# Kernel tuning notes

Hardware: AMD Instinct MI355X
Metric: run time of the kernel (lower is better)

## Reference

```python
import jax, jax.numpy as jnp
import numpy as np

B, S, D_MODEL, H = 2, 2048, 1024, 16
HD = D_MODEL // H  # 64
THETA = 10000.0


def setup_inputs() -> dict:
    key = jax.random.key(0)
    ks = jax.random.split(key, 5)
    std = (2.0 / (D_MODEL + D_MODEL)) ** 0.5
    x = jax.random.normal(ks[0], (B, S, D_MODEL), dtype=jnp.float32)
    Wq = jax.random.normal(ks[1], (D_MODEL, D_MODEL), dtype=jnp.float32) * std
    Wk = jax.random.normal(ks[2], (D_MODEL, D_MODEL), dtype=jnp.float32) * std
    Wv = jax.random.normal(ks[3], (D_MODEL, D_MODEL), dtype=jnp.float32) * std
    Wo = jax.random.normal(ks[4], (D_MODEL, D_MODEL), dtype=jnp.float32) * std
    # RoPE tables (buffers)
    pos = jnp.arange(S, dtype=jnp.float32)
    freq = THETA ** (-jnp.arange(0, HD, 2, dtype=jnp.float32) / HD)  # [HD/2]
    ang = jnp.outer(pos, freq)  # [S, HD/2]
    token_positions = jnp.arange(S, dtype=jnp.int32)
    return {
        "x": x,
        "token_positions": token_positions,
        "use_rope": 1,
        "Wq": Wq, "Wk": Wk, "Wv": Wv, "Wo": Wo,
        "cos": jnp.cos(ang), "sin": jnp.sin(ang),
    }


def _apply_rope(t, c, sn):
    # t: [b,h,s,d]; c,sn: [s,d/2] (broadcast over b,h)
    e = t[..., 0::2]
    o = t[..., 1::2]
    return jnp.stack([e * c - o * sn, o * c + e * sn], axis=-1).reshape(t.shape)


def reference(x, token_positions, use_rope, Wq, Wk, Wv, Wo, cos, sin):
    b, s, _ = x.shape

    def split_heads(t):  # [b,s,D] -> [b,h,s,hd]
        return t.reshape(b, s, H, HD).transpose(0, 2, 1, 3)

    q = split_heads(x @ Wq.T)
    k = split_heads(x @ Wk.T)
    v = split_heads(x @ Wv.T)

    if use_rope:
        c = cos[token_positions]   # [s, hd/2]
        sn = sin[token_positions]  # [s, hd/2]
        q = _apply_rope(q, c, sn)
        k = _apply_rope(k, c, sn)

    scale = 1.0 / jnp.sqrt(jnp.float32(HD))
    scores = jnp.einsum('bhqd,bhkd->bhqk', q, k) * scale  # [b,h,s,s]
    causal = jnp.tril(jnp.ones((s, s), dtype=bool))
    scores = jnp.where(causal, scores, -jnp.inf)
    attn = jax.nn.softmax(scores, axis=-1)
    y = jnp.einsum('bhqk,bhkd->bhqd', attn, v)
    y = y.transpose(0, 2, 1, 3).reshape(b, s, D_MODEL)
    return y @ Wo.T
```

## Files before the change

### kernel.cpp

```cpp
#include <hip/hip_runtime.h>
#include <math.h>

#define BB 2
#define SS 2048
#define DM 1024
#define NH 16
#define HD 64

typedef __attribute__((ext_vector_type(8))) __bf16 bf16x8;
typedef __attribute__((ext_vector_type(4))) __bf16 bf16x4;
typedef __attribute__((ext_vector_type(8))) unsigned short u16x8;
typedef __attribute__((ext_vector_type(4))) float f32x4;
typedef unsigned short u16;
typedef unsigned int u32;
typedef __attribute__((address_space(1))) unsigned int u32g;
typedef __attribute__((address_space(3))) unsigned int u32l;

#define CEXP 0.18033688011112042f

static __device__ __forceinline__ u16 f2bf(float f) {
    __bf16 h = (__bf16)f;
    return __builtin_bit_cast(unsigned short, h);
}

static __device__ __forceinline__ void gld16(const u16* g, u16* l) {
    __builtin_amdgcn_global_load_lds((const u32g*)g, (u32l*)l, 16, 0, 0);
}

__global__ __launch_bounds__(256)
void cast_all(const float* __restrict__ x,
              const float* __restrict__ wq, const float* __restrict__ wk,
              const float* __restrict__ wv, const float* __restrict__ wo,
              u16* __restrict__ xb, u16* __restrict__ wqb, u16* __restrict__ wkb,
              u16* __restrict__ wvb, u16* __restrict__ wob)
{
    const int N4X = (BB * SS * DM) / 4;
    const int N4W = (DM * DM) / 4;
    int i = blockIdx.x * 256 + threadIdx.x;
    const float* src; u16* dst; int off;
    if (i < N4X) { src = x; dst = xb; off = i; }
    else {
        int i2 = i - N4X;
        int w = i2 >> 18;
        off = i2 & (N4W - 1);
        switch (w) {
            case 0:  src = wq; dst = wqb; break;
            case 1:  src = wk; dst = wkb; break;
            case 2:  src = wv; dst = wvb; break;
            default: src = wo; dst = wob; break;
        }
    }
    float4 v = ((const float4*)src)[off];
    ushort4 o;
    o.x = f2bf(v.x); o.y = f2bf(v.y); o.z = f2bf(v.z); o.w = f2bf(v.w);
    ((ushort4*)dst)[off] = o;
}

__global__ __launch_bounds__(256)
void qkv_gemm(const u16* __restrict__ X,
              const u16* __restrict__ Wq, const u16* __restrict__ Wk,
              const u16* __restrict__ Wv,
              u16* __restrict__ Q, u16* __restrict__ K, u16* __restrict__ V)
{
    const u16* W; u16* dst;
    if (blockIdx.z == 0)      { W = Wq; dst = Q; }
    else if (blockIdx.z == 1) { W = Wk; dst = K; }
    else                      { W = Wv; dst = V; }

    __shared__ u16 As[128 * 32];
    __shared__ u16 Bs[128 * 32];
    const int t  = threadIdx.x;
    const int wv = t >> 6, L = t & 63, ln = L & 15, qd = L >> 4;
    const int i0 = blockIdx.y * 128, j0 = blockIdx.x * 128;
    const int wm = (wv >> 1) * 64, wn = (wv & 1) * 64;
    const int srow = L >> 2, scol = (L & 3) * 8;

    f32x4 acc[4][4];
    #pragma unroll
    for (int a = 0; a < 4; ++a)
        #pragma unroll
        for (int b = 0; b < 4; ++b)
            #pragma unroll
            for (int e = 0; e < 4; ++e) acc[a][b][e] = 0.f;

    for (int k0 = 0; k0 < DM; k0 += 32) {
        __syncthreads();
        gld16(X + (size_t)(i0 + wv * 32 +      srow) * DM + k0 + scol, &As[(wv * 32     ) * 32]);
        gld16(X + (size_t)(i0 + wv * 32 + 16 + srow) * DM + k0 + scol, &As[(wv * 32 + 16) * 32]);
        gld16(W + (size_t)(j0 + wv * 32 +      srow) * DM + k0 + scol, &Bs[(wv * 32     ) * 32]);
        gld16(W + (size_t)(j0 + wv * 32 + 16 + srow) * DM + k0 + scol, &Bs[(wv * 32 + 16) * 32]);
        __syncthreads();
        bf16x8 a[4], b[4];
        #pragma unroll
        for (int mi = 0; mi < 4; ++mi) a[mi] = *(const bf16x8*)&As[(wm + mi * 16 + ln) * 32 + qd * 8];
        #pragma unroll
        for (int ni = 0; ni < 4; ++ni) b[ni] = *(const bf16x8*)&Bs[(wn + ni * 16 + ln) * 32 + qd * 8];
        #pragma unroll
        for (int mi = 0; mi < 4; ++mi)
            #pragma unroll
            for (int ni = 0; ni < 4; ++ni)
                acc[mi][ni] = __builtin_amdgcn_mfma_f32_16x16x32_bf16(a[mi], b[ni], acc[mi][ni], 0, 0, 0);
    }

    #pragma unroll
    for (int mi = 0; mi < 4; ++mi)
        #pragma unroll
        for (int ni = 0; ni < 4; ++ni)
            #pragma unroll
            for (int r = 0; r < 4; ++r) {
                int gi = i0 + wm + mi * 16 + qd * 4 + r;
                int gj = j0 + wn + ni * 16 + ln;
                int b = gi >> 11, s = gi & 2047, h = gj >> 6, d = gj & 63;
                dst[(((size_t)(b * NH + h)) * SS + s) * HD + d] = f2bf(acc[mi][ni][r]);
            }
}

__global__ __launch_bounds__(256)
void out_gemm(const u16* __restrict__ X, const u16* __restrict__ W,
              float* __restrict__ dst)
{
    __shared__ u16 As[128 * 32];
    __shared__ u16 Bs[128 * 32];
    const int t  = threadIdx.x;
    const int wv = t >> 6, L = t & 63, ln = L & 15, qd = L >> 4;
    const int i0 = blockIdx.y * 128, j0 = blockIdx.x * 128;
    const int wm = (wv >> 1) * 64, wn = (wv & 1) * 64;
    const int srow = L >> 2, scol = (L & 3) * 8;

    f32x4 acc[4][4];
    #pragma unroll
    for (int a = 0; a < 4; ++a)
        #pragma unroll
        for (int b = 0; b < 4; ++b)
            #pragma unroll
            for (int e = 0; e < 4; ++e) acc[a][b][e] = 0.f;

    for (int k0 = 0; k0 < DM; k0 += 32) {
        __syncthreads();
        gld16(X + (size_t)(i0 + wv * 32 +      srow) * DM + k0 + scol, &As[(wv * 32     ) * 32]);
        gld16(X + (size_t)(i0 + wv * 32 + 16 + srow) * DM + k0 + scol, &As[(wv * 32 + 16) * 32]);
        gld16(W + (size_t)(j0 + wv * 32 +      srow) * DM + k0 + scol, &Bs[(wv * 32     ) * 32]);
        gld16(W + (size_t)(j0 + wv * 32 + 16 + srow) * DM + k0 + scol, &Bs[(wv * 32 + 16) * 32]);
        __syncthreads();
        bf16x8 a[4], b[4];
        #pragma unroll
        for (int mi = 0; mi < 4; ++mi) a[mi] = *(const bf16x8*)&As[(wm + mi * 16 + ln) * 32 + qd * 8];
        #pragma unroll
        for (int ni = 0; ni < 4; ++ni) b[ni] = *(const bf16x8*)&Bs[(wn + ni * 16 + ln) * 32 + qd * 8];
        #pragma unroll
        for (int mi = 0; mi < 4; ++mi)
            #pragma unroll
            for (int ni = 0; ni < 4; ++ni)
                acc[mi][ni] = __builtin_amdgcn_mfma_f32_16x16x32_bf16(a[mi], b[ni], acc[mi][ni], 0, 0, 0);
    }

    #pragma unroll
    for (int mi = 0; mi < 4; ++mi)
        #pragma unroll
        for (int ni = 0; ni < 4; ++ni)
            #pragma unroll
            for (int r = 0; r < 4; ++r) {
                int gi = i0 + wm + mi * 16 + qd * 4 + r;
                int gj = j0 + wn + ni * 16 + ln;
                dst[(size_t)gi * DM + gj] = acc[mi][ni][r];
            }
}

__global__ __launch_bounds__(256)
void rope_kernel(u16* __restrict__ Q, u16* __restrict__ Kt,
                 const int* __restrict__ tp, const float* __restrict__ cosp,
                 const float* __restrict__ sinp, const int* __restrict__ use_rope)
{
    if (use_rope[0] == 0) return;
    int idx = blockIdx.x * 256 + threadIdx.x;
    int p = idx & 31, s = (idx >> 5) & 2047, bh = idx >> 16;
    int pos = tp[s];
    float c  = cosp[pos * 32 + p];
    float sn = sinp[pos * 32 + p];
    size_t base = ((size_t)bh * SS + s) * HD + 2 * p;
    u32 qw = *(u32*)&Q[base];
    u32 kw = *(u32*)&Kt[base];
    float qe = __uint_as_float(qw << 16), qo = __uint_as_float(qw & 0xffff0000u);
    float ke = __uint_as_float(kw << 16), ko = __uint_as_float(kw & 0xffff0000u);
    u32 qn = (u32)f2bf(qe * c - qo * sn) | ((u32)f2bf(qo * c + qe * sn) << 16);
    u32 kn = (u32)f2bf(ke * c - ko * sn) | ((u32)f2bf(ko * c + ke * sn) << 16);
    *(u32*)&Q[base]  = qn;
    *(u32*)&Kt[base] = kn;
}

static __device__ __forceinline__ void group_step(
    const bf16x8 af[4][2], const bf16x8 qf[2], u16* psw,
    int diag, int rowg, int j0, int ln, int qd,
    float& m, float& l, f32x4* o, bf16x8& pf0, bf16x8& pf1)
{
    f32x4 s[4];
    #pragma unroll
    for (int mt = 0; mt < 4; ++mt) {
        #pragma unroll
        for (int e = 0; e < 4; ++e) s[mt][e] = 0.f;
        s[mt] = __builtin_amdgcn_mfma_f32_16x16x32_bf16(af[mt][0], qf[0], s[mt], 0, 0, 0);
        s[mt] = __builtin_amdgcn_mfma_f32_16x16x32_bf16(af[mt][1], qf[1], s[mt], 0, 0, 0);
    }
    if (diag) {
        #pragma unroll
        for (int mt = 0; mt < 4; ++mt)
            #pragma unroll
            for (int r = 0; r < 4; ++r)
                if (j0 + mt * 16 + qd * 4 + r > rowg) s[mt][r] = -3.0e38f;
    }
    float rm = s[0][0];
    #pragma unroll
    for (int mt = 0; mt < 4; ++mt)
        #pragma unroll
        for (int r = 0; r < 4; ++r) rm = fmaxf(rm, s[mt][r]);
    rm = fmaxf(rm, __shfl_xor(rm, 16));
    rm = fmaxf(rm, __shfl_xor(rm, 32));
    float nm = fmaxf(m, rm);
    float alpha = exp2f((m - nm) * CEXP);
    float nmc = nm * CEXP;
    float rs = 0.f;
    #pragma unroll
    for (int mt = 0; mt < 4; ++mt) {
        bf16x4 pk;
        #pragma unroll
        for (int r = 0; r < 4; ++r) {
            float pv = exp2f(fmaf(s[mt][r], CEXP, -nmc));
            rs += pv;
            pk[r] = (__bf16)pv;
        }
        *(bf16x4*)(psw + ln * 72 + mt * 16 + qd * 4) = pk;
    }
    rs += __shfl_xor(rs, 16);
    rs += __shfl_xor(rs, 32);
    l = l * alpha + rs;
    m = nm;
    #pragma unroll
    for (int r = 0; r < 4; ++r) {
        float ar = __shfl(alpha, qd * 4 + r);
        #pragma unroll
        for (int ni = 0; ni < 4; ++ni) o[ni][r] *= ar;
    }
    pf0 = *(const bf16x8*)(psw + ln * 72 + qd * 8);
    pf1 = *(const bf16x8*)(psw + ln * 72 + 32 + qd * 8);
}

__global__ __launch_bounds__(256, 2)
void attn_kernel(const u16* __restrict__ Q, const u16* __restrict__ K,
                 const u16* __restrict__ V, u16* __restrict__ Y)
{
    __shared__ u16 Ks[64 * 64];
    __shared__ u16 Vt[64 * 64];
    __shared__ u16 Ps[4][2][16 * 72];

    const int t  = threadIdx.x;
    const int wv = t >> 6, L = t & 63, ln = L & 15, qd = L >> 4;
    const int bh = blockIdx.x, p = blockIdx.y;
    const int qbA = p * 64, qbB = (31 - p) * 64;
    const u16* Qp = Q + (size_t)bh * SS * HD;
    const u16* Kp = K + (size_t)bh * SS * HD;
    const u16* Vp = V + (size_t)bh * SS * HD;

    bf16x8 qfA[2], qfB[2];
    {
        const u16* ra = Qp + (size_t)(qbA + wv * 16 + ln) * HD;
        qfA[0] = *(const bf16x8*)(ra + qd * 8);
        qfA[1] = *(const bf16x8*)(ra + 32 + qd * 8);
        const u16* rb = Qp + (size_t)(qbB + wv * 16 + ln) * HD;
        qfB[0] = *(const bf16x8*)(rb + qd * 8);
        qfB[1] = *(const bf16x8*)(rb + 32 + qd * 8);
    }

    f32x4 oA[4], oB[4];
    #pragma unroll
    for (int ni = 0; ni < 4; ++ni)
        #pragma unroll
        for (int e = 0; e < 4; ++e) { oA[ni][e] = 0.f; oB[ni][e] = 0.f; }
    float mA = -3.0e38f, lA = 0.f, mB = -3.0e38f, lB = 0.f;

    const int ntile = 32 - p;
    for (int tix = 0; tix < ntile; ++tix) {
        const int j0 = tix * 64;
        __syncthreads();
        #pragma unroll
        for (int cc = 0; cc < 2; ++cc) {
            int c = t + cc * 256;
            int kr = c >> 3, c8 = c & 7;
            u16x8 val = *(const u16x8*)(Kp + (size_t)(j0 + kr) * HD + c8 * 8);
            *(u16x8*)&Ks[kr * 64 + ((c8 ^ (kr & 7)) * 8)] = val;
        }
        {
            int kp = t & 31, dg = t >> 5;
            const u16* v0 = Vp + (size_t)(j0 + 2 * kp) * HD + dg * 8;
            u16x8 va = *(const u16x8*)v0;
            u16x8 vb = *(const u16x8*)(v0 + HD);
            #pragma unroll
            for (int u = 0; u < 8; ++u) {
                int d = dg * 8 + u;
                u32 w = (u32)va[u] | ((u32)vb[u] << 16);
                *(u32*)&Vt[d * 64 + ((kp >> 2) ^ (d & 7)) * 8 + 2 * (kp & 3)] = w;
            }
        }
        __syncthreads();

        bf16x8 af[4][2];
        #pragma unroll
        for (int mt = 0; mt < 4; ++mt)
            #pragma unroll
            for (int kc = 0; kc < 2; ++kc)
                af[mt][kc] = *(const bf16x8*)&Ks[(mt * 16 + ln) * 64 + (((kc * 4 + qd) ^ (ln & 7)) * 8)];

        const bool hasA = (tix <= p);
        bf16x8 pA0, pA1, pB0, pB1;
        if (hasA)
            group_step(af, qfA, &Ps[wv][0][0], tix == p, qbA + wv * 16 + ln, j0, ln, qd,
                       mA, lA, oA, pA0, pA1);
        group_step(af, qfB, &Ps[wv][1][0], tix == ntile - 1, qbB + wv * 16 + ln, j0, ln, qd,
                   mB, lB, oB, pB0, pB1);

        #pragma unroll
        for (int kc = 0; kc < 2; ++kc)
            #pragma unroll
            for (int ni = 0; ni < 4; ++ni) {
                bf16x8 vf = *(const bf16x8*)&Vt[(ni * 16 + ln) * 64 + (((kc * 4 + qd) ^ (ln & 7)) * 8)];
                if (hasA)
                    oA[ni] = __builtin_amdgcn_mfma_f32_16x16x32_bf16(kc ? pA1 : pA0, vf, oA[ni], 0, 0, 0);
                oB[ni] = __builtin_amdgcn_mfma_f32_16x16x32_bf16(kc ? pB1 : pB0, vf, oB[ni], 0, 0, 0);
            }
    }

    const int b = bh >> 4, h = bh & 15;
    #pragma unroll
    for (int r = 0; r < 4; ++r) {
        float invA = 1.f / __shfl(lA, qd * 4 + r);
        float invB = 1.f / __shfl(lB, qd * 4 + r);
        int sA = qbA + wv * 16 + qd * 4 + r;
        int sB = qbB + wv * 16 + qd * 4 + r;
        #pragma unroll
        for (int ni = 0; ni < 4; ++ni) {
            int d = ni * 16 + ln;
            Y[((size_t)(b * SS + sA)) * DM + h * HD + d] = f2bf(oA[ni][r] * invA);
            Y[((size_t)(b * SS + sB)) * DM + h * HD + d] = f2bf(oB[ni][r] * invB);
        }
    }
}

extern "C" void kernel_launch(void* const* d_in, const int* in_sizes, int n_in,
                              void* d_out, int out_size, void* d_ws, size_t ws_size,
                              hipStream_t stream)
{
    const float* x        = (const float*)d_in[0];
    const int*   tp       = (const int*)d_in[1];
    const int*   use_rope = (const int*)d_in[2];
    const float* Wq       = (const float*)d_in[3];
    const float* Wk       = (const float*)d_in[4];
    const float* Wv       = (const float*)d_in[5];
    const float* Wo       = (const float*)d_in[6];
    const float* cosp     = (const float*)d_in[7];
    const float* sinp     = (const float*)d_in[8];
    float* out = (float*)d_out;

    char* ws = (char*)d_ws;
    const size_t MB = 1 << 20;
    u16* xb  = (u16*)(ws);
    u16* Wqb = (u16*)(ws + 8 * MB);
    u16* Wkb = (u16*)(ws + 10 * MB);
    u16* Wvb = (u16*)(ws + 12 * MB);
    u16* Wob = (u16*)(ws + 14 * MB);
    u16* Qb  = (u16*)(ws + 16 * MB);
    u16* Kb  = (u16*)(ws + 24 * MB);
    u16* Vb  = (u16*)(ws + 32 * MB);
    u16* Yb  = (u16*)(ws + 40 * MB);

    cast_all<<<8192, 256, 0, stream>>>(x, Wq, Wk, Wv, Wo, xb, Wqb, Wkb, Wvb, Wob);
    qkv_gemm<<<dim3(DM / 128, BB * SS / 128, 3), 256, 0, stream>>>(xb, Wqb, Wkb, Wvb, Qb, Kb, Vb);
    rope_kernel<<<(BB * NH * SS * 32) / 256, 256, 0, stream>>>(Qb, Kb, tp, cosp, sinp, use_rope);
    attn_kernel<<<dim3(BB * NH, 16), 256, 0, stream>>>(Qb, Kb, Vb, Yb);
    out_gemm<<<dim3(DM / 128, BB * SS / 128), 256, 0, stream>>>(Yb, Wob, out);
}
```

Baseline: 211.0 us.

## Fuse RoPE into QKV GEMM epilogue and use K=64 swizzled LDS tiles

Removes the separate rope kernel by applying the rotation in the QKV GEMM epilogue, getting the partner element through a lane shuffle. This avoids a full read and write pass over Q and K. Both GEMMs now stage K=64 slices per iteration with an XOR-swizzled LDS layout, which halves the number of barrier pairs and is meant to avoid LDS bank conflicts. Launch bounds now request 2 blocks per SIMD. The trade-off is double the LDS footprint and possible register pressure, plus scattered cos/sin loads in the epilogue.

```diff
diff --git a/kernel.cpp b/kernel.cpp
--- a/kernel.cpp
+++ b/kernel.cpp
@@ -56,10 +56,12 @@
     ((ushort4*)dst)[off] = o;
 }
 
-__global__ __launch_bounds__(256)
+__global__ __launch_bounds__(256, 2)
 void qkv_gemm(const u16* __restrict__ X,
               const u16* __restrict__ Wq, const u16* __restrict__ Wk,
               const u16* __restrict__ Wv,
+              const int* __restrict__ tp, const float* __restrict__ cosp,
+              const float* __restrict__ sinp, const int* __restrict__ use_rope,
               u16* __restrict__ Q, u16* __restrict__ K, u16* __restrict__ V)
 {
     const u16* W; u16* dst;
@@ -67,13 +69,14 @@
     else if (blockIdx.z == 1) { W = Wk; dst = K; }
     else                      { W = Wv; dst = V; }
 
-    __shared__ u16 As[128 * 32];
-    __shared__ u16 Bs[128 * 32];
+    __shared__ u16 As[128 * 64];
+    __shared__ u16 Bs[128 * 64];
     const int t  = threadIdx.x;
     const int wv = t >> 6, L = t & 63, ln = L & 15, qd = L >> 4;
     const int i0 = blockIdx.y * 128, j0 = blockIdx.x * 128;
     const int wm = (wv >> 1) * 64, wn = (wv & 1) * 64;
-    const int srow = L >> 2, scol = (L & 3) * 8;
+    const int srow = L >> 3;
+    const int scg  = ((L & 7) ^ (L >> 3)) * 8;
 
     f32x4 acc[4][4];
     #pragma unroll
@@ -83,49 +86,72 @@
             #pragma unroll
             for (int e = 0; e < 4; ++e) acc[a][b][e] = 0.f;
 
-    for (int k0 = 0; k0 < DM; k0 += 32) {
-        __syncthreads();
-        gld16(X + (size_t)(i0 + wv * 32 +      srow) * DM + k0 + scol, &As[(wv * 32     ) * 32]);
-        gld16(X + (size_t)(i0 + wv * 32 + 16 + srow) * DM + k0 + scol, &As[(wv * 32 + 16) * 32]);
-        gld16(W + (size_t)(j0 + wv * 32 +      srow) * DM + k0 + scol, &Bs[(wv * 32     ) * 32]);
-        gld16(W + (size_t)(j0 + wv * 32 + 16 + srow) * DM + k0 + scol, &Bs[(wv * 32 + 16) * 32]);
-        __syncthreads();
-        bf16x8 a[4], b[4];
-        #pragma unroll
-        for (int mi = 0; mi < 4; ++mi) a[mi] = *(const bf16x8*)&As[(wm + mi * 16 + ln) * 32 + qd * 8];
-        #pragma unroll
-        for (int ni = 0; ni < 4; ++ni) b[ni] = *(const bf16x8*)&Bs[(wn + ni * 16 + ln) * 32 + qd * 8];
+    for (int k0 = 0; k0 < DM; k0 += 64) {
+        __syncthreads();
+        #pragma unroll
+        for (int g = 0; g < 4; ++g) {
+            int rb = wv * 32 + g * 8;
+            gld16(X + (size_t)(i0 + rb + srow) * DM + k0 + scg, &As[rb * 64]);
+            gld16(W + (size_t)(j0 + rb + srow) * DM + k0 + scg, &Bs[rb * 64]);
+        }
+        __syncthreads();
+        bf16x8 a[4][2], b[4][2];
         #pragma unroll
         for (int mi = 0; mi < 4; ++mi)
             #pragma unroll
-            for (int ni = 0; ni < 4; ++ni)
-                acc[mi][ni] = __builtin_amdgcn_mfma_f32_16x16x32_bf16(a[mi], b[ni], acc[mi][ni], 0, 0, 0);
-    }
-
+            for (int kd = 0; kd < 2; ++kd)
+                a[mi][kd] = *(const bf16x8*)&As[(wm + mi * 16 + ln) * 64 + (((kd * 4 + qd) ^ (ln & 7)) * 8)];
+        #pragma unroll
+        for (int ni = 0; ni < 4; ++ni)
+            #pragma unroll
+            for (int kd = 0; kd < 2; ++kd)
+                b[ni][kd] = *(const bf16x8*)&Bs[(wn + ni * 16 + ln) * 64 + (((kd * 4 + qd) ^ (ln & 7)) * 8)];
+        #pragma unroll
+        for (int kd = 0; kd < 2; ++kd)
+            #pragma unroll
+            for (int mi = 0; mi < 4; ++mi)
+                #pragma unroll
+                for (int ni = 0; ni < 4; ++ni)
+                    acc[mi][ni] = __builtin_amdgcn_mfma_f32_16x16x32_bf16(a[mi][kd], b[ni][kd], acc[mi][ni], 0, 0, 0);
+    }
+
+    const int rope_on = (blockIdx.z < 2) ? use_rope[0] : 0;
     #pragma unroll
     for (int mi = 0; mi < 4; ++mi)
         #pragma unroll
-        for (int ni = 0; ni < 4; ++ni)
-            #pragma unroll
-            for (int r = 0; r < 4; ++r) {
-                int gi = i0 + wm + mi * 16 + qd * 4 + r;
+        for (int r = 0; r < 4; ++r) {
+            int gi = i0 + wm + mi * 16 + qd * 4 + r;
+            int b_ = gi >> 11, s = gi & 2047;
+            int pos = tp[s];
+            #pragma unroll
+            for (int ni = 0; ni < 4; ++ni) {
                 int gj = j0 + wn + ni * 16 + ln;
-                int b = gi >> 11, s = gi & 2047, h = gj >> 6, d = gj & 63;
-                dst[(((size_t)(b * NH + h)) * SS + s) * HD + d] = f2bf(acc[mi][ni][r]);
+                int h = gj >> 6, d = gj & 63;
+                float v = acc[mi][ni][r];
+                float pv = __shfl_xor(v, 1);
+                if (rope_on) {
+                    int p = d >> 1;
+                    float c  = cosp[pos * 32 + p];
+                    float sn = sinp[pos * 32 + p];
+                    v = (d & 1) ? (v * c + pv * sn) : (v * c - pv * sn);
+                }
+                dst[(((size_t)(b_ * NH + h)) * SS + s) * HD + d] = f2bf(v);
             }
-}
-
-__global__ __launch_bounds__(256)
+        }
+}
+
+__global__ __launch_bounds__(256, 2)
 void out_gemm(const u16* __restrict__ X, const u16* __restrict__ W,
               float* __restrict__ dst)
 {
-    __shared__ u16 As[128 * 32];
-    __shared__ u16 Bs[128 * 32];
+    __shared__ u16 As[128 * 64];
+    __shared__ u16 Bs[128 * 64];
     const int t  = threadIdx.x;
     const int wv = t >> 6, L = t & 63, ln = L & 15, qd = L >> 4;
     const int i0 = blockIdx.y * 128, j0 = blockIdx.x * 128;
     const int wm = (wv >> 1) * 64, wn = (wv & 1) * 64;
-    const int srow = L >> 2, scol = (L & 3) * 8;
+    const int srow = L >> 3;
+    const int scg  = ((L & 7) ^ (L >> 3)) * 8;
 
     f32x4 acc[4][4];
     #pragma unroll
@@ -135,23 +161,33 @@
             #pragma unroll
             for (int e = 0; e < 4; ++e) acc[a][b][e] = 0.f;
 
-    for (int k0 = 0; k0 < DM; k0 += 32) {
-        __syncthreads();
-        gld16(X + (size_t)(i0 + wv * 32 +      srow) * DM + k0 + scol, &As[(wv * 32     ) * 32]);
-        gld16(X + (size_t)(i0 + wv * 32 + 16 + srow) * DM + k0 + scol, &As[(wv * 32 + 16) * 32]);
-        gld16(W + (size_t)(j0 + wv * 32 +      srow) * DM + k0 + scol, &Bs[(wv * 32     ) * 32]);
-        gld16(W + (size_t)(j0 + wv * 32 + 16 + srow) * DM + k0 + scol, &Bs[(wv * 32 + 16) * 32]);
-        __syncthreads();
-        bf16x8 a[4], b[4];
-        #pragma unroll
-        for (int mi = 0; mi < 4; ++mi) a[mi] = *(const bf16x8*)&As[(wm + mi * 16 + ln) * 32 + qd * 8];
-        #pragma unroll
-        for (int ni = 0; ni < 4; ++ni) b[ni] = *(const bf16x8*)&Bs[(wn + ni * 16 + ln) * 32 + qd * 8];
+    for (int k0 = 0; k0 < DM; k0 += 64) {
+        __syncthreads();
+        #pragma unroll
+        for (int g = 0; g < 4; ++g) {
+            int rb = wv * 32 + g * 8;
+            gld16(X + (size_t)(i0 + rb + srow) * DM + k0 + scg, &As[rb * 64]);
+            gld16(W + (size_t)(j0 + rb + srow) * DM + k0 + scg, &Bs[rb * 64]);
+        }
+        __syncthreads();
+        bf16x8 a[4][2], b[4][2];
         #pragma unroll
         for (int mi = 0; mi < 4; ++mi)
             #pragma unroll
-            for (int ni = 0; ni < 4; ++ni)
-                acc[mi][ni] = __builtin_amdgcn_mfma_f32_16x16x32_bf16(a[mi], b[ni], acc[mi][ni], 0, 0, 0);
+            for (int kd = 0; kd < 2; ++kd)
+                a[mi][kd] = *(const bf16x8*)&As[(wm + mi * 16 + ln) * 64 + (((kd * 4 + qd) ^ (ln & 7)) * 8)];
+        #pragma unroll
+        for (int ni = 0; ni < 4; ++ni)
+            #pragma unroll
+            for (int kd = 0; kd < 2; ++kd)
+                b[ni][kd] = *(const bf16x8*)&Bs[(wn + ni * 16 + ln) * 64 + (((kd * 4 + qd) ^ (ln & 7)) * 8)];
+        #pragma unroll
+        for (int kd = 0; kd < 2; ++kd)
+            #pragma unroll
+            for (int mi = 0; mi < 4; ++mi)
+                #pragma unroll
+                for (int ni = 0; ni < 4; ++ni)
+                    acc[mi][ni] = __builtin_amdgcn_mfma_f32_16x16x32_bf16(a[mi][kd], b[ni][kd], acc[mi][ni], 0, 0, 0);
     }
 
     #pragma unroll
@@ -164,28 +200,6 @@
                 int gj = j0 + wn + ni * 16 + ln;
                 dst[(size_t)gi * DM + gj] = acc[mi][ni][r];
             }
-}
-
-__global__ __launch_bounds__(256)
-void rope_kernel(u16* __restrict__ Q, u16* __restrict__ Kt,
-                 const int* __restrict__ tp, const float* __restrict__ cosp,
-                 const float* __restrict__ sinp, const int* __restrict__ use_rope)
-{
-    if (use_rope[0] == 0) return;
-    int idx = blockIdx.x * 256 + threadIdx.x;
-    int p = idx & 31, s = (idx >> 5) & 2047, bh = idx >> 16;
-    int pos = tp[s];
-    float c  = cosp[pos * 32 + p];
-    float sn = sinp[pos * 32 + p];
-    size_t base = ((size_t)bh * SS + s) * HD + 2 * p;
-    u32 qw = *(u32*)&Q[base];
-    u32 kw = *(u32*)&Kt[base];
-    float qe = __uint_as_float(qw << 16), qo = __uint_as_float(qw & 0xffff0000u);
-    float ke = __uint_as_float(kw << 16), ko = __uint_as_float(kw & 0xffff0000u);
-    u32 qn = (u32)f2bf(qe * c - qo * sn) | ((u32)f2bf(qo * c + qe * sn) << 16);
-    u32 kn = (u32)f2bf(ke * c - ko * sn) | ((u32)f2bf(ko * c + ke * sn) << 16);
-    *(u32*)&Q[base]  = qn;
-    *(u32*)&Kt[base] = kn;
 }
 
 static __device__ __forceinline__ void group_step(
@@ -372,8 +386,8 @@
     u16* Yb  = (u16*)(ws + 40 * MB);
 
     cast_all<<<8192, 256, 0, stream>>>(x, Wq, Wk, Wv, Wo, xb, Wqb, Wkb, Wvb, Wob);
-    qkv_gemm<<<dim3(DM / 128, BB * SS / 128, 3), 256, 0, stream>>>(xb, Wqb, Wkb, Wvb, Qb, Kb, Vb);
-    rope_kernel<<<(BB * NH * SS * 32) / 256, 256, 0, stream>>>(Qb, Kb, tp, cosp, sinp, use_rope);
+    qkv_gemm<<<dim3(DM / 128, BB * SS / 128, 3), 256, 0, stream>>>(
+        xb, Wqb, Wkb, Wvb, tp, cosp, sinp, use_rope, Qb, Kb, Vb);
     attn_kernel<<<dim3(BB * NH, 16), 256, 0, stream>>>(Qb, Kb, Vb, Yb);
     out_gemm<<<dim3(DM / 128, BB * SS / 128), 256, 0, stream>>>(Yb, Wob, out);
 }
```

Measured after the change: 201.3 us. 4.6% less time.
